# Kernel optimization log

Measured on AMD Instinct MI355X. Metric: run time of the kernel, lower is better.

## Reference

```python
import jax, jax.numpy as jnp
import numpy as np

N_NODES = 100000
N_CELLS = 200000
N_EDGES = 300000
D = 128            # input_size == attention_size
HID = 128          # hidden width of custom_func MLP
SCALE = np.sqrt(np.float32(D))


def segment_softmax(src, seg_ids, num_segments):
    # src: [M, 1], seg_ids: [M] -> softmax normalized within each segment
    m = jax.ops.segment_max(src, seg_ids, num_segments=num_segments)
    e = jnp.exp(src - m[seg_ids])
    s = jax.ops.segment_sum(e, seg_ids, num_segments=num_segments)
    return e / s[seg_ids]


def setup_inputs() -> dict:
    key = jax.random.key(0)
    ks = jax.random.split(key, 9)
    cell_attr = jax.random.normal(ks[0], (N_CELLS, D), dtype=jnp.float32)
    edge_attr = jax.random.normal(ks[1], (N_EDGES, D), dtype=jnp.float32)
    node_embedding = jax.random.normal(ks[2], (N_NODES, D), dtype=jnp.float32)
    edge_index = jax.random.randint(ks[3], (2, N_EDGES), 0, N_NODES, dtype=jnp.int32)
    face = jax.random.randint(ks[4], (3, N_CELLS), 0, N_NODES, dtype=jnp.int32)
    # custom_func: 2-layer MLP (2D -> HID -> D)
    W1 = jax.random.normal(ks[5], (2 * D, HID), dtype=jnp.float32) / np.sqrt(2 * D)
    b1 = jnp.zeros((HID,), dtype=jnp.float32)
    W2 = jax.random.normal(ks[6], (HID, D), dtype=jnp.float32) / np.sqrt(HID)
    b2 = jnp.zeros((D,), dtype=jnp.float32)
    return {"cell_attr": cell_attr, "edge_attr": edge_attr,
            "node_embedding": node_embedding, "edge_index": edge_index,
            "face": face, "W1": W1, "b1": b1, "W2": W2, "b2": b2}


def reference(cell_attr, edge_attr, node_embedding, edge_index, face, W1, b1, W2, b2):
    senders, receivers = edge_index[0], edge_index[1]
    two_out = jnp.concatenate([receivers, senders], axis=0)   # outdegree order [2E]
    two_edge = jnp.concatenate([edge_attr, edge_attr], axis=0)  # [2E, D]

    # attention over edges grouped by target (outdegree) node
    att_src = jnp.sum(two_edge * node_embedding[two_out], axis=1, keepdims=True) / SCALE
    att = segment_softmax(att_src, two_out, N_NODES)            # [2E, 1]
    node_agg = jax.ops.segment_sum(two_edge * att, two_out, num_segments=N_NODES)  # [N, D]

    # cells gather mean of their 3 nodes
    cell_agg = (node_agg[face[0]] + node_agg[face[1]] + node_agg[face[2]]) / 3.0  # [C, D]

    # custom_func MLP on cat(cell_attr, cell_agg)
    h = jax.nn.relu(jnp.concatenate([cell_attr, cell_agg], axis=1) @ W1 + b1)
    cell_attr_new = h @ W2 + b2                                  # [C, D]

    # scatter_mean of cell features back to nodes
    cells_node_index = jnp.concatenate([face[0], face[1], face[2]], axis=0)  # [3C]
    tripled = jnp.concatenate([cell_attr_new] * 3, axis=0)                   # [3C, D]
    sums = jax.ops.segment_sum(tripled, cells_node_index, num_segments=N_NODES)
    counts = jax.ops.segment_sum(jnp.ones((3 * N_CELLS,), jnp.float32),
                                 cells_node_index, num_segments=N_NODES)
    node_attr = sums / jnp.maximum(counts, 1.0)[:, None]

    return cell_attr_new, node_attr
```

## Files before the change

### kernel.cpp

```cpp
#include <hip/hip_runtime.h>

#define NN 100000
#define NC 200000
#define NE 300000
#define D  128
#define NB 391
#define ATT_B 2048
#define HB 2344

typedef unsigned short u16;
typedef __attribute__((ext_vector_type(8))) short bf16x8;
typedef __attribute__((ext_vector_type(4))) float f32x4;

__device__ __forceinline__ u16 f2bf(float x) {
    unsigned int u = __float_as_uint(x);
    u += 0x7fffu + ((u >> 16) & 1u);
    return (u16)(u >> 16);
}
__device__ __forceinline__ float bf2f(u16 h) {
    return __uint_as_float((unsigned int)h << 16);
}
__device__ __forceinline__ unsigned int cvt_pk_bf16(float a, float b) {
    unsigned int r;
    asm("v_cvt_pk_bf16_f32 %0, %1, %2" : "=v"(r) : "v"(a), "v"(b));
    return r;
}

#define MFMA16(a, b, c) __builtin_amdgcn_mfma_f32_16x16x32_bf16((a), (b), (c), 0, 0, 0)

__global__ __launch_bounds__(256) void k_att(const float* __restrict__ edge_attr,
                                             const float* __restrict__ emb,
                                             const int* __restrict__ ei,
                                             float* __restrict__ expv,
                                             int* __restrict__ cntA) {
    const int HW = ATT_B * 8;
    int hw  = blockIdx.x * 8 + (threadIdx.x >> 5);
    int sub = threadIdx.x & 31;
    const float inv_scale = 0.08838834764831845f;
    for (int e0 = hw; e0 < NE; e0 += 2 * HW) {
        int e1 = e0 + HW;
        bool h1 = (e1 < NE);
        int sd0 = ei[e0], rc0 = ei[NE + e0];
        int sd1 = h1 ? ei[e1] : 0;
        int rc1 = h1 ? ei[NE + e1] : 0;
        float4 a0 = ((const float4*)(edge_attr + (size_t)e0 * D))[sub];
        float4 r0 = ((const float4*)(emb + (size_t)rc0 * D))[sub];
        float4 s0 = ((const float4*)(emb + (size_t)sd0 * D))[sub];
        float dr0 = a0.x * r0.x + a0.y * r0.y + a0.z * r0.z + a0.w * r0.w;
        float ds0 = a0.x * s0.x + a0.y * s0.y + a0.z * s0.z + a0.w * s0.w;
        float dr1 = 0.f, ds1 = 0.f;
        if (h1) {
            float4 a1 = ((const float4*)(edge_attr + (size_t)e1 * D))[sub];
            float4 r1 = ((const float4*)(emb + (size_t)rc1 * D))[sub];
            float4 s1 = ((const float4*)(emb + (size_t)sd1 * D))[sub];
            dr1 = a1.x * r1.x + a1.y * r1.y + a1.z * r1.z + a1.w * r1.w;
            ds1 = a1.x * s1.x + a1.y * s1.y + a1.z * s1.z + a1.w * s1.w;
        }
        #pragma unroll
        for (int off = 16; off > 0; off >>= 1) {
            dr0 += __shfl_xor(dr0, off);
            ds0 += __shfl_xor(ds0, off);
            dr1 += __shfl_xor(dr1, off);
            ds1 += __shfl_xor(ds1, off);
        }
        if (sub == 0) {
            expv[e0]      = __expf(dr0 * inv_scale);
            expv[NE + e0] = __expf(ds0 * inv_scale);
            atomicAdd(&cntA[rc0], 1);
            atomicAdd(&cntA[sd0], 1);
            if (h1) {
                expv[e1]      = __expf(dr1 * inv_scale);
                expv[NE + e1] = __expf(ds1 * inv_scale);
                atomicAdd(&cntA[rc1], 1);
                atomicAdd(&cntA[sd1], 1);
            }
        }
    }
}

__global__ __launch_bounds__(256) void k_prep_face_w(const int* __restrict__ face,
                                                     int* __restrict__ cntF,
                                                     const float* __restrict__ W1,
                                                     const float* __restrict__ W2,
                                                     u16* __restrict__ w1h, u16* __restrict__ w1l,
                                                     u16* __restrict__ w2h, u16* __restrict__ w2l) {
    int b = blockIdx.x;
    int t = threadIdx.x;
    if (b < HB) {
        int i = b * 256 + t;
        if (i >= 3 * NC) return;
        atomicAdd(&cntF[face[i]], 1);
    } else {
        int tid = (b - HB) * 256 + t;
        if (tid >= 6144) return;
        int l = tid & 63;
        int f = tid >> 6;
        const float* W; u16 *oh, *ol; int fi;
        if (f < 64) { W = W1; oh = w1h; ol = w1l; fi = f; }
        else        { W = W2; oh = w2h; ol = w2l; fi = f - 64; }
        int kt = fi >> 3, nt = fi & 7;
        int k0 = kt * 32 + 8 * (l >> 4);
        int n  = nt * 16 + (l & 15);
        #pragma unroll
        for (int i = 0; i < 8; i++) {
            float x = W[(size_t)(k0 + i) * 128 + n];
            u16 h = f2bf(x);
            oh[(size_t)fi * 512 + l * 8 + i] = h;
            ol[(size_t)fi * 512 + l * 8 + i] = f2bf(x - bf2f(h));
        }
    }
}

__global__ __launch_bounds__(256) void k_scan_blocks(const int* __restrict__ cntA,
                                                     const int* __restrict__ cntF,
                                                     int* __restrict__ bsumA,
                                                     int* __restrict__ bsumF) {
    __shared__ int s[256];
    int bb = blockIdx.x;
    bool fa = bb >= NB;
    const int* cnt = fa ? cntF : cntA;
    int* bsum = fa ? bsumF : bsumA;
    int blk = fa ? bb - NB : bb;
    int t = threadIdx.x;
    int i = blk * 256 + t;
    s[t] = (i < NN) ? cnt[i] : 0;
    __syncthreads();
    #pragma unroll
    for (int off = 128; off > 0; off >>= 1) {
        if (t < off) s[t] += s[t + off];
        __syncthreads();
    }
    if (t == 0) bsum[blk] = s[0];
}

__global__ __launch_bounds__(512) void k_scan_top(int* __restrict__ bsumA,
                                                  int* __restrict__ bsumF, int nb) {
    __shared__ int s[512];
    int* bsum = blockIdx.x ? bsumF : bsumA;
    int t = threadIdx.x;
    int v = (t < nb) ? bsum[t] : 0;
    s[t] = v;
    __syncthreads();
    #pragma unroll
    for (int off = 1; off < 512; off <<= 1) {
        int x = (t >= off) ? s[t - off] : 0;
        __syncthreads();
        s[t] += x;
        __syncthreads();
    }
    if (t < nb) bsum[t] = s[t] - v;
}

__global__ __launch_bounds__(256) void k_scan_final(const int* __restrict__ cntA,
                                                    const int* __restrict__ cntF,
                                                    const int* __restrict__ bsumA,
                                                    const int* __restrict__ bsumF,
                                                    int* __restrict__ offA,
                                                    int* __restrict__ offF) {
    __shared__ int s[256];
    int bb = blockIdx.x;
    bool fa = bb >= NB;
    const int* cnt = fa ? cntF : cntA;
    const int* bsum = fa ? bsumF : bsumA;
    int* off_out = fa ? offF : offA;
    int total = fa ? 3 * NC : 2 * NE;
    int blk = fa ? bb - NB : bb;
    int t = threadIdx.x;
    int i = blk * 256 + t;
    int v = (i < NN) ? cnt[i] : 0;
    s[t] = v;
    __syncthreads();
    #pragma unroll
    for (int off = 1; off < 256; off <<= 1) {
        int x = (t >= off) ? s[t - off] : 0;
        __syncthreads();
        s[t] += x;
        __syncthreads();
    }
    if (i < NN) off_out[i] = s[t] - v + bsum[blk];
    if (i == 0) off_out[NN] = total;
}

__global__ __launch_bounds__(256) void k_fill(const int* __restrict__ ei,
                                              const float* __restrict__ expv,
                                              const int* __restrict__ face,
                                              const int* __restrict__ offA,
                                              const int* __restrict__ offF,
                                              int* __restrict__ curA,
                                              int* __restrict__ curF,
                                              int2* __restrict__ swA,
                                              int* __restrict__ slotsF) {
    int b = blockIdx.x;
    int t = threadIdx.x;
    if (b < HB) {
        int i = b * 256 + t;
        if (i >= 2 * NE) return;
        int tgt = (i < NE) ? ei[NE + i] : ei[i - NE];
        int pos = offA[tgt] + atomicAdd(&curA[tgt], 1);
        int2 p;
        p.x = (i < NE) ? i : i - NE;
        p.y = __float_as_int(expv[i]);
        swA[pos] = p;
    } else {
        int i = (b - HB) * 256 + t;
        if (i >= 3 * NC) return;
        int tgt = face[i];
        int pos = offF[tgt] + atomicAdd(&curF[tgt], 1);
        int c = i; if (c >= NC) c -= NC; if (c >= NC) c -= NC;
        slotsF[pos] = c;
    }
}

__global__ __launch_bounds__(256) void k_agg_gather(const float* __restrict__ edge_attr,
                                                    const int2* __restrict__ swA,
                                                    const int* __restrict__ offs,
                                                    float* __restrict__ na) {
    int n = blockIdx.x * 4 + (threadIdx.x >> 6);
    int lane = threadIdx.x & 63;
    if (n >= NN) return;
    int s0 = offs[n], s1 = offs[n + 1];
    int deg = s1 - s0;
    float2 acc = {0.f, 0.f};
    float wsum = 0.f;
    int base = 0;
    while (base < deg) {
        int chunk = deg - base;
        if (chunk > 64) chunk = 64;
        int sl = 0; float wl = 0.f;
        if (lane < chunk) {
            int2 p = swA[s0 + base + lane];
            sl = p.x;
            wl = __int_as_float(p.y);
        }
        wsum += wl;
        int j = 0;
        for (; j + 4 <= chunk; j += 4) {
            int r0 = __shfl(sl, j),     r1 = __shfl(sl, j + 1);
            int r2 = __shfl(sl, j + 2), r3 = __shfl(sl, j + 3);
            float w0 = __shfl(wl, j),     w1 = __shfl(wl, j + 1);
            float w2 = __shfl(wl, j + 2), w3 = __shfl(wl, j + 3);
            float2 a0 = ((const float2*)(edge_attr + (size_t)r0 * D))[lane];
            float2 a1 = ((const float2*)(edge_attr + (size_t)r1 * D))[lane];
            float2 a2 = ((const float2*)(edge_attr + (size_t)r2 * D))[lane];
            float2 a3 = ((const float2*)(edge_attr + (size_t)r3 * D))[lane];
            acc.x += w0 * a0.x + w1 * a1.x + w2 * a2.x + w3 * a3.x;
            acc.y += w0 * a0.y + w1 * a1.y + w2 * a2.y + w3 * a3.y;
        }
        for (; j < chunk; ++j) {
            int rr = __shfl(sl, j);
            float ww = __shfl(wl, j);
            float2 a = ((const float2*)(edge_attr + (size_t)rr * D))[lane];
            acc.x += ww * a.x;
            acc.y += ww * a.y;
        }
        base += chunk;
    }
    #pragma unroll
    for (int off = 32; off > 0; off >>= 1) wsum += __shfl_xor(wsum, off);
    float inv = (deg > 0) ? 1.f / wsum : 0.f;
    float2 r; r.x = acc.x * inv; r.y = acc.y * inv;
    ((float2*)(na + (size_t)n * D))[lane] = r;
}

__global__ __launch_bounds__(256) void k_smean_gather(const float* __restrict__ cell_out,
                                                      const int* __restrict__ offs,
                                                      const int* __restrict__ slots,
                                                      float* __restrict__ node_out) {
    int n = blockIdx.x * 4 + (threadIdx.x >> 6);
    int lane = threadIdx.x & 63;
    if (n >= NN) return;
    int s0 = offs[n], s1 = offs[n + 1];
    int deg = s1 - s0;
    float2 acc = {0.f, 0.f};
    int base = 0;
    while (base < deg) {
        int chunk = deg - base;
        if (chunk > 64) chunk = 64;
        int sl = 0;
        if (lane < chunk) sl = slots[s0 + base + lane];
        int j = 0;
        for (; j + 4 <= chunk; j += 4) {
            int c0 = __shfl(sl, j),     c1 = __shfl(sl, j + 1);
            int c2 = __shfl(sl, j + 2), c3 = __shfl(sl, j + 3);
            float2 y0 = ((const float2*)(cell_out + (size_t)c0 * D))[lane];
            float2 y1 = ((const float2*)(cell_out + (size_t)c1 * D))[lane];
            float2 y2 = ((const float2*)(cell_out + (size_t)c2 * D))[lane];
            float2 y3 = ((const float2*)(cell_out + (size_t)c3 * D))[lane];
            acc.x += y0.x + y1.x + y2.x + y3.x;
            acc.y += y0.y + y1.y + y2.y + y3.y;
        }
        for (; j < chunk; ++j) {
            int cc = __shfl(sl, j);
            float2 y = ((const float2*)(cell_out + (size_t)cc * D))[lane];
            acc.x += y.x;
            acc.y += y.y;
        }
        base += chunk;
    }
    int degc = s1 - s0;
    float inv = degc ? 1.f / (float)degc : 0.f;
    float2 r; r.x = acc.x * inv; r.y = acc.y * inv;
    ((float2*)(node_out + (size_t)n * D))[lane] = r;
}

__device__ __forceinline__ void stage_split(char* lds, int row, int col8, const float* v) {
    unsigned int byte = ((unsigned int)row << 9) + ((unsigned int)col8 << 4);
    byte ^= (unsigned int)(row & 7) << 4;
    uint4 hi, lo;
    unsigned int* hp = (unsigned int*)&hi;
    unsigned int* lp = (unsigned int*)&lo;
    #pragma unroll
    for (int i = 0; i < 4; i++) {
        unsigned int h = cvt_pk_bf16(v[2 * i], v[2 * i + 1]);
        float h0 = __uint_as_float(h << 16);
        float h1 = __uint_as_float(h & 0xffff0000u);
        hp[i] = h;
        lp[i] = cvt_pk_bf16(v[2 * i] - h0, v[2 * i + 1] - h1);
    }
    *(uint4*)(lds + byte)         = hi;
    *(uint4*)(lds + 16384 + byte) = lo;
}

__global__ __launch_bounds__(256, 4) void k_mlp(const float* __restrict__ cell_attr,
                                                const float* __restrict__ na,
                                                const int* __restrict__ face,
                                                const u16* __restrict__ w1h,
                                                const u16* __restrict__ w1l,
                                                const u16* __restrict__ w2h,
                                                const u16* __restrict__ w2l,
                                                const float* __restrict__ b1,
                                                const float* __restrict__ b2,
                                                float* __restrict__ out) {
    __shared__ char lds[32768];
    const int t  = threadIdx.x;
    const int c0 = blockIdx.x * 32;

    {
        const int r = t >> 3;
        const int q = t & 7;
        float v[16];
        const float* pa = cell_attr + (size_t)(c0 + r) * D + q * 16;
        #pragma unroll
        for (int i = 0; i < 4; i++) *(float4*)(v + 4 * i) = *(const float4*)(pa + 4 * i);
        stage_split(lds, r, q * 2,     v);
        stage_split(lds, r, q * 2 + 1, v + 8);

        const int cid = c0 + r;
        const int f0 = face[cid], f1 = face[NC + cid], f2 = face[2 * NC + cid];
        const float* p0 = na + (size_t)f0 * D + q * 16;
        const float* p1 = na + (size_t)f1 * D + q * 16;
        const float* p2 = na + (size_t)f2 * D + q * 16;
        const float third = 1.f / 3.f;
        #pragma unroll
        for (int i = 0; i < 4; i++) {
            float4 a0 = *(const float4*)(p0 + 4 * i);
            float4 a1 = *(const float4*)(p1 + 4 * i);
            float4 a2 = *(const float4*)(p2 + 4 * i);
            v[4 * i + 0] = (a0.x + a1.x + a2.x) * third;
            v[4 * i + 1] = (a0.y + a1.y + a2.y) * third;
            v[4 * i + 2] = (a0.z + a1.z + a2.z) * third;
            v[4 * i + 3] = (a0.w + a1.w + a2.w) * third;
        }
        stage_split(lds, r, 16 + q * 2, v);
        stage_split(lds, r, 17 + q * 2, v + 8);
    }
    __syncthreads();

    const int w  = t >> 6;
    const int l  = t & 63;
    const int lr = l & 15;
    const int lg = l >> 4;
    const unsigned int swz = (unsigned int)(lr & 7) << 4;
    const size_t wl8 = (size_t)l * 8;
    const f32x4 z4 = {0.f, 0.f, 0.f, 0.f};
    f32x4 acc[2][2] = {{z4, z4}, {z4, z4}};

    {
        const unsigned int abase = ((unsigned int)lr << 9) + ((unsigned int)lg << 4);
        const u16* pW1h = w1h + (size_t)(w * 2) * 512 + wl8;
        const u16* pW1l = w1l + (size_t)(w * 2) * 512 + wl8;
        #pragma unroll 2
        for (int kt = 0; kt < 8; ++kt) {
            unsigned int ab = (abase + (unsigned int)kt * 64) ^ swz;
            bf16x8 aH0 = *(const bf16x8*)(lds + ab);
            bf16x8 aL0 = *(const bf16x8*)(lds + 16384 + ab);
            bf16x8 aH1 = *(const bf16x8*)(lds + ab + 8192);
            bf16x8 aL1 = *(const bf16x8*)(lds + 16384 + ab + 8192);
            #pragma unroll
            for (int jn = 0; jn < 2; ++jn) {
                size_t fo = (size_t)(kt * 8 + jn) * 512;
                bf16x8 bH = *(const bf16x8*)(pW1h + fo);
                bf16x8 bL = *(const bf16x8*)(pW1l + fo);
                acc[0][jn] = MFMA16(aH0, bL, acc[0][jn]);
                acc[0][jn] = MFMA16(aL0, bH, acc[0][jn]);
                acc[0][jn] = MFMA16(aH0, bH, acc[0][jn]);
                acc[1][jn] = MFMA16(aH1, bL, acc[1][jn]);
                acc[1][jn] = MFMA16(aL1, bH, acc[1][jn]);
                acc[1][jn] = MFMA16(aH1, bH, acc[1][jn]);
            }
        }
    }

    __syncthreads();

    {
        const int col0 = w * 32 + lr;
        const int col1 = col0 + 16;
        const float bb0 = b1[col0];
        const float bb1 = b1[col1];
        #pragma unroll
        for (int rt = 0; rt < 2; ++rt) {
            #pragma unroll
            for (int r = 0; r < 4; ++r) {
                int row = rt * 16 + lg * 4 + r;
                float h0 = fmaxf(acc[rt][0][r] + bb0, 0.f);
                float h1 = fmaxf(acc[rt][1][r] + bb1, 0.f);
                unsigned int ph = cvt_pk_bf16(h0, h1);
                float f0 = __uint_as_float(ph << 16);
                float f1 = __uint_as_float(ph & 0xffff0000u);
                unsigned int pl = cvt_pk_bf16(h0 - f0, h1 - f1);
                unsigned int swzr = (unsigned int)(row & 7) << 4;
                unsigned int b0 = (((unsigned int)row << 8) + ((unsigned int)col0 << 1)) ^ swzr;
                unsigned int bcol1 = (((unsigned int)row << 8) + ((unsigned int)col1 << 1)) ^ swzr;
                *(u16*)(lds + b0)            = (u16)ph;
                *(u16*)(lds + bcol1)         = (u16)(ph >> 16);
                *(u16*)(lds + 8192 + b0)     = (u16)pl;
                *(u16*)(lds + 8192 + bcol1)  = (u16)(pl >> 16);
            }
        }
    }
    __syncthreads();

    f32x4 acc2[2][2] = {{z4, z4}, {z4, z4}};
    {
        const unsigned int abase = ((unsigned int)lr << 8) + ((unsigned int)lg << 4);
        const u16* pW2h = w2h + (size_t)(w * 2) * 512 + wl8;
        const u16* pW2l = w2l + (size_t)(w * 2) * 512 + wl8;
        #pragma unroll 2
        for (int kt = 0; kt < 4; ++kt) {
            unsigned int ab = (abase + (unsigned int)kt * 64) ^ swz;
            bf16x8 aH0 = *(const bf16x8*)(lds + ab);
            bf16x8 aL0 = *(const bf16x8*)(lds + 8192 + ab);
            bf16x8 aH1 = *(const bf16x8*)(lds + ab + 4096);
            bf16x8 aL1 = *(const bf16x8*)(lds + 8192 + ab + 4096);
            #pragma unroll
            for (int jn = 0; jn < 2; ++jn) {
                size_t fo = (size_t)(kt * 8 + jn) * 512;
                bf16x8 bH = *(const bf16x8*)(pW2h + fo);
                bf16x8 bL = *(const bf16x8*)(pW2l + fo);
                acc2[0][jn] = MFMA16(aH0, bL, acc2[0][jn]);
                acc2[0][jn] = MFMA16(aL0, bH, acc2[0][jn]);
                acc2[0][jn] = MFMA16(aH0, bH, acc2[0][jn]);
                acc2[1][jn] = MFMA16(aH1, bL, acc2[1][jn]);
                acc2[1][jn] = MFMA16(aL1, bH, acc2[1][jn]);
                acc2[1][jn] = MFMA16(aH1, bH, acc2[1][jn]);
            }
        }
    }

    #pragma unroll
    for (int jn = 0; jn < 2; ++jn) {
        int col = w * 32 + jn * 16 + lr;
        float bb = b2[col];
        #pragma unroll
        for (int rt = 0; rt < 2; ++rt) {
            #pragma unroll
            for (int r = 0; r < 4; ++r) {
                int row = c0 + rt * 16 + lg * 4 + r;
                out[(size_t)row * D + col] = acc2[rt][jn][r] + bb;
            }
        }
    }
}

extern "C" void kernel_launch(void* const* d_in, const int* in_sizes, int n_in,
                              void* d_out, int out_size, void* d_ws, size_t ws_size,
                              hipStream_t stream) {
    (void)in_sizes; (void)n_in; (void)out_size; (void)ws_size;
    const float* cell_attr = (const float*)d_in[0];
    const float* edge_attr = (const float*)d_in[1];
    const float* emb       = (const float*)d_in[2];
    const int*   ei        = (const int*)d_in[3];
    const int*   face      = (const int*)d_in[4];
    const float* W1        = (const float*)d_in[5];
    const float* b1        = (const float*)d_in[6];
    const float* W2        = (const float*)d_in[7];
    const float* b2        = (const float*)d_in[8];

    float* out_cell = (float*)d_out;
    float* out_node = out_cell + (size_t)NC * D;

    int*   cntA   = (int*)d_ws;
    int*   cntF   = cntA + NN;
    int*   curA   = cntF + NN;
    int*   curF   = curA + NN;
    float* expv   = (float*)(curF + NN);
    int*   offA   = (int*)(expv + 2 * NE);
    int*   offF   = offA + NN + 1;
    int*   bsumA  = offF + NN + 1;
    int*   bsumF  = bsumA + 512;
    int*   slotsF = bsumF + 512;
    int2*  swA    = (int2*)(((uintptr_t)(slotsF + 3 * NC) + 7) & ~(uintptr_t)7);
    u16* w1h = (u16*)(((uintptr_t)(swA + 2 * NE) + 15) & ~(uintptr_t)15);
    u16* w1l = w1h + 64 * 512;
    u16* w2h = w1l + 64 * 512;
    u16* w2l = w2h + 32 * 512;

    hipMemsetAsync(d_ws, 0, (size_t)4 * NN * 4, stream);

    k_att<<<ATT_B, 256, 0, stream>>>(edge_attr, emb, ei, expv, cntA);

    k_prep_face_w<<<HB + 24, 256, 0, stream>>>(face, cntF, W1, W2, w1h, w1l, w2h, w2l);

    k_scan_blocks<<<2 * NB, 256, 0, stream>>>(cntA, cntF, bsumA, bsumF);
    k_scan_top   <<<2, 512, 0, stream>>>(bsumA, bsumF, NB);
    k_scan_final <<<2 * NB, 256, 0, stream>>>(cntA, cntF, bsumA, bsumF, offA, offF);

    k_fill<<<2 * HB, 256, 0, stream>>>(ei, expv, face, offA, offF, curA, curF, swA, slotsF);

    k_agg_gather<<<(NN + 3) / 4, 256, 0, stream>>>(edge_attr, swA, offA, out_node);

    k_mlp<<<NC / 32, 256, 0, stream>>>(cell_attr, out_node, face,
                                       w1h, w1l, w2h, w2l, b1, b2, out_cell);

    k_smean_gather<<<(NN + 3) / 4, 256, 0, stream>>>(out_cell, offF, slotsF, out_node);
}
```

Baseline: 658.1 us.

## Fuse attention score computation into per-node aggregation gather

Drops the separate edge-attention kernel. Attention logits are now computed inside the per-node gather, using that node's embedding loaded once and the edge_attr row already fetched for aggregation. This removes a full pass that read edge_attr plus two gathered embedding rows per edge and wrote an exp buffer, and the slot array shrinks from int2 to int. In exchange the gather kernel does a 64-lane shuffle reduction and an exp for every edge, which adds latency inside the dependent loop. The MLP launch-bounds occupancy hint also goes from 4 to 5.

```diff
diff --git a/kernel.cpp b/kernel.cpp
--- a/kernel.cpp
+++ b/kernel.cpp
@@ -5,7 +5,6 @@
 #define NE 300000
 #define D  128
 #define NB 391
-#define ATT_B 2048
 #define HB 2344
 
 typedef unsigned short u16;
@@ -28,70 +27,27 @@
 
 #define MFMA16(a, b, c) __builtin_amdgcn_mfma_f32_16x16x32_bf16((a), (b), (c), 0, 0, 0)
 
-__global__ __launch_bounds__(256) void k_att(const float* __restrict__ edge_attr,
-                                             const float* __restrict__ emb,
-                                             const int* __restrict__ ei,
-                                             float* __restrict__ expv,
-                                             int* __restrict__ cntA) {
-    const int HW = ATT_B * 8;
-    int hw  = blockIdx.x * 8 + (threadIdx.x >> 5);
-    int sub = threadIdx.x & 31;
-    const float inv_scale = 0.08838834764831845f;
-    for (int e0 = hw; e0 < NE; e0 += 2 * HW) {
-        int e1 = e0 + HW;
-        bool h1 = (e1 < NE);
-        int sd0 = ei[e0], rc0 = ei[NE + e0];
-        int sd1 = h1 ? ei[e1] : 0;
-        int rc1 = h1 ? ei[NE + e1] : 0;
-        float4 a0 = ((const float4*)(edge_attr + (size_t)e0 * D))[sub];
-        float4 r0 = ((const float4*)(emb + (size_t)rc0 * D))[sub];
-        float4 s0 = ((const float4*)(emb + (size_t)sd0 * D))[sub];
-        float dr0 = a0.x * r0.x + a0.y * r0.y + a0.z * r0.z + a0.w * r0.w;
-        float ds0 = a0.x * s0.x + a0.y * s0.y + a0.z * s0.z + a0.w * s0.w;
-        float dr1 = 0.f, ds1 = 0.f;
-        if (h1) {
-            float4 a1 = ((const float4*)(edge_attr + (size_t)e1 * D))[sub];
-            float4 r1 = ((const float4*)(emb + (size_t)rc1 * D))[sub];
-            float4 s1 = ((const float4*)(emb + (size_t)sd1 * D))[sub];
-            dr1 = a1.x * r1.x + a1.y * r1.y + a1.z * r1.z + a1.w * r1.w;
-            ds1 = a1.x * s1.x + a1.y * s1.y + a1.z * s1.z + a1.w * s1.w;
-        }
-        #pragma unroll
-        for (int off = 16; off > 0; off >>= 1) {
-            dr0 += __shfl_xor(dr0, off);
-            ds0 += __shfl_xor(ds0, off);
-            dr1 += __shfl_xor(dr1, off);
-            ds1 += __shfl_xor(ds1, off);
-        }
-        if (sub == 0) {
-            expv[e0]      = __expf(dr0 * inv_scale);
-            expv[NE + e0] = __expf(ds0 * inv_scale);
-            atomicAdd(&cntA[rc0], 1);
-            atomicAdd(&cntA[sd0], 1);
-            if (h1) {
-                expv[e1]      = __expf(dr1 * inv_scale);
-                expv[NE + e1] = __expf(ds1 * inv_scale);
-                atomicAdd(&cntA[rc1], 1);
-                atomicAdd(&cntA[sd1], 1);
-            }
-        }
-    }
-}
-
-__global__ __launch_bounds__(256) void k_prep_face_w(const int* __restrict__ face,
-                                                     int* __restrict__ cntF,
-                                                     const float* __restrict__ W1,
-                                                     const float* __restrict__ W2,
-                                                     u16* __restrict__ w1h, u16* __restrict__ w1l,
-                                                     u16* __restrict__ w2h, u16* __restrict__ w2l) {
+__global__ __launch_bounds__(256) void k_hist_w(const int* __restrict__ ei,
+                                                const int* __restrict__ face,
+                                                int* __restrict__ cntA,
+                                                int* __restrict__ cntF,
+                                                const float* __restrict__ W1,
+                                                const float* __restrict__ W2,
+                                                u16* __restrict__ w1h, u16* __restrict__ w1l,
+                                                u16* __restrict__ w2h, u16* __restrict__ w2l) {
     int b = blockIdx.x;
     int t = threadIdx.x;
     if (b < HB) {
         int i = b * 256 + t;
+        if (i >= 2 * NE) return;
+        int tgt = (i < NE) ? ei[NE + i] : ei[i - NE];
+        atomicAdd(&cntA[tgt], 1);
+    } else if (b < 2 * HB) {
+        int i = (b - HB) * 256 + t;
         if (i >= 3 * NC) return;
         atomicAdd(&cntF[face[i]], 1);
     } else {
-        int tid = (b - HB) * 256 + t;
+        int tid = (b - 2 * HB) * 256 + t;
         if (tid >= 6144) return;
         int l = tid & 63;
         int f = tid >> 6;
@@ -182,13 +138,12 @@
 }
 
 __global__ __launch_bounds__(256) void k_fill(const int* __restrict__ ei,
-                                              const float* __restrict__ expv,
                                               const int* __restrict__ face,
                                               const int* __restrict__ offA,
                                               const int* __restrict__ offF,
                                               int* __restrict__ curA,
                                               int* __restrict__ curF,
-                                              int2* __restrict__ swA,
+                                              int* __restrict__ slotsA,
                                               int* __restrict__ slotsF) {
     int b = blockIdx.x;
     int t = threadIdx.x;
@@ -197,10 +152,7 @@
         if (i >= 2 * NE) return;
         int tgt = (i < NE) ? ei[NE + i] : ei[i - NE];
         int pos = offA[tgt] + atomicAdd(&curA[tgt], 1);
-        int2 p;
-        p.x = (i < NE) ? i : i - NE;
-        p.y = __float_as_int(expv[i]);
-        swA[pos] = p;
+        slotsA[pos] = (i < NE) ? i : i - NE;
     } else {
         int i = (b - HB) * 256 + t;
         if (i >= 3 * NC) return;
@@ -211,52 +163,65 @@
     }
 }
 
-__global__ __launch_bounds__(256) void k_agg_gather(const float* __restrict__ edge_attr,
-                                                    const int2* __restrict__ swA,
-                                                    const int* __restrict__ offs,
-                                                    float* __restrict__ na) {
+__global__ __launch_bounds__(256) void k_agg_att(const float* __restrict__ edge_attr,
+                                                 const float* __restrict__ emb,
+                                                 const int* __restrict__ offs,
+                                                 const int* __restrict__ slots,
+                                                 float* __restrict__ na) {
     int n = blockIdx.x * 4 + (threadIdx.x >> 6);
     int lane = threadIdx.x & 63;
     if (n >= NN) return;
     int s0 = offs[n], s1 = offs[n + 1];
     int deg = s1 - s0;
+    float2 e = ((const float2*)(emb + (size_t)n * D))[lane];
+    const float inv_scale = 0.08838834764831845f;
     float2 acc = {0.f, 0.f};
     float wsum = 0.f;
     int base = 0;
     while (base < deg) {
         int chunk = deg - base;
         if (chunk > 64) chunk = 64;
-        int sl = 0; float wl = 0.f;
-        if (lane < chunk) {
-            int2 p = swA[s0 + base + lane];
-            sl = p.x;
-            wl = __int_as_float(p.y);
-        }
-        wsum += wl;
+        int sl = (lane < chunk) ? slots[s0 + base + lane] : 0;
         int j = 0;
         for (; j + 4 <= chunk; j += 4) {
             int r0 = __shfl(sl, j),     r1 = __shfl(sl, j + 1);
             int r2 = __shfl(sl, j + 2), r3 = __shfl(sl, j + 3);
-            float w0 = __shfl(wl, j),     w1 = __shfl(wl, j + 1);
-            float w2 = __shfl(wl, j + 2), w3 = __shfl(wl, j + 3);
             float2 a0 = ((const float2*)(edge_attr + (size_t)r0 * D))[lane];
             float2 a1 = ((const float2*)(edge_attr + (size_t)r1 * D))[lane];
             float2 a2 = ((const float2*)(edge_attr + (size_t)r2 * D))[lane];
             float2 a3 = ((const float2*)(edge_attr + (size_t)r3 * D))[lane];
+            float d0 = a0.x * e.x + a0.y * e.y;
+            float d1 = a1.x * e.x + a1.y * e.y;
+            float d2 = a2.x * e.x + a2.y * e.y;
+            float d3 = a3.x * e.x + a3.y * e.y;
+            #pragma unroll
+            for (int off = 32; off > 0; off >>= 1) {
+                d0 += __shfl_xor(d0, off);
+                d1 += __shfl_xor(d1, off);
+                d2 += __shfl_xor(d2, off);
+                d3 += __shfl_xor(d3, off);
+            }
+            float w0 = __expf(d0 * inv_scale);
+            float w1 = __expf(d1 * inv_scale);
+            float w2 = __expf(d2 * inv_scale);
+            float w3 = __expf(d3 * inv_scale);
             acc.x += w0 * a0.x + w1 * a1.x + w2 * a2.x + w3 * a3.x;
             acc.y += w0 * a0.y + w1 * a1.y + w2 * a2.y + w3 * a3.y;
+            wsum += (w0 + w1) + (w2 + w3);
         }
         for (; j < chunk; ++j) {
             int rr = __shfl(sl, j);
-            float ww = __shfl(wl, j);
             float2 a = ((const float2*)(edge_attr + (size_t)rr * D))[lane];
-            acc.x += ww * a.x;
-            acc.y += ww * a.y;
+            float d = a.x * e.x + a.y * e.y;
+            #pragma unroll
+            for (int off = 32; off > 0; off >>= 1) d += __shfl_xor(d, off);
+            float w = __expf(d * inv_scale);
+            acc.x += w * a.x;
+            acc.y += w * a.y;
+            wsum += w;
         }
         base += chunk;
     }
-    #pragma unroll
-    for (int off = 32; off > 0; off >>= 1) wsum += __shfl_xor(wsum, off);
     float inv = (deg > 0) ? 1.f / wsum : 0.f;
     float2 r; r.x = acc.x * inv; r.y = acc.y * inv;
     ((float2*)(na + (size_t)n * D))[lane] = r;
@@ -297,8 +262,7 @@
         }
         base += chunk;
     }
-    int degc = s1 - s0;
-    float inv = degc ? 1.f / (float)degc : 0.f;
+    float inv = deg ? 1.f / (float)deg : 0.f;
     float2 r; r.x = acc.x * inv; r.y = acc.y * inv;
     ((float2*)(node_out + (size_t)n * D))[lane] = r;
 }
@@ -321,7 +285,7 @@
     *(uint4*)(lds + 16384 + byte) = lo;
 }
 
-__global__ __launch_bounds__(256, 4) void k_mlp(const float* __restrict__ cell_attr,
+__global__ __launch_bounds__(256, 5) void k_mlp(const float* __restrict__ cell_attr,
                                                 const float* __restrict__ na,
                                                 const int* __restrict__ face,
                                                 const u16* __restrict__ w1h,
@@ -494,31 +458,29 @@
     int*   cntF   = cntA + NN;
     int*   curA   = cntF + NN;
     int*   curF   = curA + NN;
-    float* expv   = (float*)(curF + NN);
-    int*   offA   = (int*)(expv + 2 * NE);
+    int*   offA   = curF + NN;
     int*   offF   = offA + NN + 1;
     int*   bsumA  = offF + NN + 1;
     int*   bsumF  = bsumA + 512;
-    int*   slotsF = bsumF + 512;
-    int2*  swA    = (int2*)(((uintptr_t)(slotsF + 3 * NC) + 7) & ~(uintptr_t)7);
-    u16* w1h = (u16*)(((uintptr_t)(swA + 2 * NE) + 15) & ~(uintptr_t)15);
+    int*   slotsA = bsumF + 512;
+    int*   slotsF = slotsA + 2 * NE;
+    u16* w1h = (u16*)(((uintptr_t)(slotsF + 3 * NC) + 15) & ~(uintptr_t)15);
     u16* w1l = w1h + 64 * 512;
     u16* w2h = w1l + 64 * 512;
     u16* w2l = w2h + 32 * 512;
 
     hipMemsetAsync(d_ws, 0, (size_t)4 * NN * 4, stream);
 
-    k_att<<<ATT_B, 256, 0, stream>>>(edge_attr, emb, ei, expv, cntA);
-
-    k_prep_face_w<<<HB + 24, 256, 0, stream>>>(face, cntF, W1, W2, w1h, w1l, w2h, w2l);
+    k_hist_w<<<2 * HB + 24, 256, 0, stream>>>(ei, face, cntA, cntF, W1, W2,
+                                              w1h, w1l, w2h, w2l);
 
     k_scan_blocks<<<2 * NB, 256, 0, stream>>>(cntA, cntF, bsumA, bsumF);
     k_scan_top   <<<2, 512, 0, stream>>>(bsumA, bsumF, NB);
     k_scan_final <<<2 * NB, 256, 0, stream>>>(cntA, cntF, bsumA, bsumF, offA, offF);
 
-    k_fill<<<2 * HB, 256, 0, stream>>>(ei, expv, face, offA, offF, curA, curF, swA, slotsF);
-
-    k_agg_gather<<<(NN + 3) / 4, 256, 0, stream>>>(edge_attr, swA, offA, out_node);
+    k_fill<<<2 * HB, 256, 0, stream>>>(ei, face, offA, offF, curA, curF, slotsA, slotsF);
+
+    k_agg_att<<<(NN + 3) / 4, 256, 0, stream>>>(edge_attr, emb, offA, slotsA, out_node);
 
     k_mlp<<<NC / 32, 256, 0, stream>>>(cell_attr, out_node, face,
                                        w1h, w1l, w2h, w2l, b1, b2, out_cell);
```

New measurement: 639.6 us. 1.03x faster.
